# Kernel tuning notes

Measured on AMD Instinct MI355X. Metric: run time of the kernel, lower is better.

The kernel has to match this reference:

```python
import jax, jax.numpy as jnp
import numpy as np

D_MODEL = 2048
N_HEADS = 16
HEAD_DIM = D_MODEL // N_HEADS  # 128
SCALE_BASE = 512


def rotate_half(x):
    x1, x2 = jnp.split(x, 2, axis=-1)
    return jnp.concatenate((-x2, x1), axis=-1)


def rotary_xpos(seq_len, dim, dtype=jnp.float32):
    inv_freq = 1.0 / (10000.0 ** (jnp.arange(0, dim, 2, dtype=jnp.float32) / dim))
    t = jnp.arange(seq_len, dtype=jnp.float32)
    freqs = jnp.einsum('i,j->ij', t, inv_freq)
    freqs = jnp.concatenate((freqs, freqs), axis=-1)  # [S, dim]
    scale_base = (jnp.arange(0, dim, 2, dtype=jnp.float32) + 0.4 * dim) / (1.4 * dim)
    power = (t - seq_len // 2) / SCALE_BASE
    scale = scale_base[None, :] ** power[:, None]  # [S, dim/2]
    scale = jnp.concatenate((scale, scale), axis=-1)  # [S, dim]
    return freqs.astype(dtype), scale.astype(dtype)


def apply_rotary(t, pos, scale):
    return t * jnp.cos(pos) * scale + rotate_half(t) * jnp.sin(pos) * scale


def setup_inputs() -> dict:
    key = jax.random.key(0)
    ks = jax.random.split(key, 5)
    B, S = 2, 2048
    hidden_states = jax.random.normal(ks[0], (B, S, D_MODEL), dtype=jnp.float32)
    # Linear weights stored as [out, in] like torch; we use x @ W.T
    w_q = jax.random.normal(ks[1], (N_HEADS * HEAD_DIM, D_MODEL), dtype=jnp.float32) * 0.02
    w_kv = jax.random.normal(ks[2], (2 * HEAD_DIM, D_MODEL), dtype=jnp.float32) * 0.02
    w_proj = jax.random.normal(ks[3], (D_MODEL, N_HEADS * HEAD_DIM), dtype=jnp.float32) * 0.02
    b_proj = jax.random.normal(ks[4], (D_MODEL,), dtype=jnp.float32) * 0.02
    return {"hidden_states": hidden_states, "w_q": w_q, "w_kv": w_kv,
            "w_proj": w_proj, "b_proj": b_proj}


def reference(hidden_states, w_q, w_kv, w_proj, b_proj):
    B, S, _ = hidden_states.shape
    q = hidden_states @ w_q.T                      # [B,S,H*D]
    kv = hidden_states @ w_kv.T                    # [B,S,2*D]
    k, v = jnp.split(kv, 2, axis=-1)               # [B,S,D] each
    q = q.reshape(B, S, N_HEADS, HEAD_DIM).transpose(0, 2, 1, 3)  # [B,H,S,D]

    scale_w = HEAD_DIM ** (-0.5)
    q = q * scale_w
    k = k * scale_w

    pos, xscale = rotary_xpos(S, HEAD_DIM, q.dtype)
    q = apply_rotary(q, pos, xscale)               # broadcast [S,D] over [B,H,S,D]
    k = apply_rotary(k, pos, 1.0 / xscale)         # [B,S,D]

    attn = jnp.einsum('bnih,bjh->bnij', q, k)      # [B,H,S,S]
    causal = jnp.triu(jnp.ones((S, S), dtype=bool), 1)
    attn = jnp.where(causal, -jnp.finfo(attn.dtype).max, attn)
    attn = jax.nn.softmax(attn, axis=-1)

    out = jnp.einsum('bnij,bjd->bind', attn, v)    # [B,S,H,D]
    out = out.reshape(B, S, N_HEADS * HEAD_DIM)
    out = out @ w_proj.T + b_proj
    return out
```

## Files before the change

kernel.cpp:

```cpp
#include <hip/hip_runtime.h>
#include <math.h>

typedef __bf16 bf16;
typedef __bf16 bf16x8 __attribute__((ext_vector_type(8)));
typedef float f32x4 __attribute__((ext_vector_type(4)));

#define MFMA16(a, b, c) __builtin_amdgcn_mfma_f32_16x16x32_bf16((a), (b), (c), 0, 0, 0)

__device__ __forceinline__ float clampf(float v, float lo, float hi) {
  return fminf(fmaxf(v, lo), hi);
}

__device__ __forceinline__ void async_copy16(const void* g, void* l) {
  __builtin_amdgcn_global_load_lds(
      (__attribute__((address_space(1))) void*)g,
      (__attribute__((address_space(3))) void*)l,
      16, 0, 0);
}


__global__ void convert_bf16(const float* __restrict__ hs,
                             const float* __restrict__ wq,
                             const float* __restrict__ wkv,
                             const float* __restrict__ wproj,
                             bf16* __restrict__ hs_bf,
                             bf16* __restrict__ wqkv_bf,
                             bf16* __restrict__ wproj_bf) {
  const long long v = (long long)blockIdx.x * blockDim.x + threadIdx.x;
  const float* src;
  bf16* dst;
  long long off;
  if (v < 1048576) { src = hs; dst = hs_bf; off = v; }
  else if (v < 1572864) { src = wq; dst = wqkv_bf; off = v - 1048576; }
  else if (v < 1638400) { src = wkv; dst = wqkv_bf + 4194304; off = v - 1572864; }
  else { src = wproj; dst = wproj_bf; off = v - 1638400; }
  const f32x4* p = (const f32x4*)(src + off * 8);
  f32x4 f0 = p[0], f1 = p[1];
  bf16x8 r;
#pragma unroll
  for (int i = 0; i < 4; ++i) { r[i] = (bf16)f0[i]; r[i + 4] = (bf16)f1[i]; }
  *(bf16x8*)(dst + off * 8) = r;
}

__global__ __launch_bounds__(256, 2)
void gemm_qkv(const bf16* __restrict__ A, const bf16* __restrict__ Bw,
              bf16* __restrict__ Cq, bf16* __restrict__ Ckv) {
  const int K = 2048;
  __shared__ bf16 As[128 * 32];
  __shared__ bf16 Bs[128 * 32];
  const int tid = threadIdx.x;
  const int wave = tid >> 6, lane = tid & 63;
  const int quad = lane >> 4, l15 = lane & 15;
  const int r4 = lane >> 2, c4 = lane & 3;
  const int wm = wave >> 1, wn = wave & 1;
  const int bm = blockIdx.y * 128;
  const int bx = blockIdx.x;
  const bf16* Bp = Bw + (size_t)bx * 128 * K;

  const f32x4 vzero = {0.f, 0.f, 0.f, 0.f};
  f32x4 acc[4][4];
#pragma unroll
  for (int i = 0; i < 4; ++i)
#pragma unroll
    for (int j = 0; j < 4; ++j) acc[i][j] = vzero;

  for (int kt = 0; kt < K; kt += 32) {
    __syncthreads();
#pragma unroll
    for (int q = 0; q < 2; ++q) {
      const int chunk = wave * 2 + q;
      const int row = chunk * 16 + r4;
      async_copy16(A + (size_t)(bm + row) * K + kt + c4 * 8, (char*)As + chunk * 1024);
      async_copy16(Bp + (size_t)row * K + kt + c4 * 8, (char*)Bs + chunk * 1024);
    }
    __syncthreads();
    bf16x8 af[4], bfr[4];
#pragma unroll
    for (int i = 0; i < 4; ++i)
      af[i] = *(const bf16x8*)((const char*)As + (wm * 64 + i * 16 + l15) * 64 + quad * 16);
#pragma unroll
    for (int i = 0; i < 4; ++i)
      bfr[i] = *(const bf16x8*)((const char*)Bs + (wn * 64 + i * 16 + l15) * 64 + quad * 16);
#pragma unroll
    for (int mi = 0; mi < 4; ++mi)
#pragma unroll
      for (int ni = 0; ni < 4; ++ni)
        acc[mi][ni] = MFMA16(af[mi], bfr[ni], acc[mi][ni]);
  }

  bf16* Cp;
  int ldc, cn;
  if (bx < 16) { Cp = Cq; ldc = 2048; cn = bx * 128; }
  else { Cp = Ckv; ldc = 256; cn = (bx - 16) * 128; }
#pragma unroll
  for (int mi = 0; mi < 4; ++mi)
#pragma unroll
    for (int ni = 0; ni < 4; ++ni) {
      const int col = cn + wn * 64 + ni * 16 + l15;
#pragma unroll
      for (int r = 0; r < 4; ++r) {
        const int row = bm + wm * 64 + mi * 16 + quad * 4 + r;
        Cp[(size_t)row * ldc + col] = (bf16)clampf(acc[mi][ni][r], -1000.f, 1000.f);
      }
    }
}

__global__ __launch_bounds__(256, 2)
void gemm_proj(const bf16* __restrict__ A, const bf16* __restrict__ Bw,
               const float* __restrict__ bias, float* __restrict__ C) {
  const int K = 2048;
  __shared__ bf16 As[128 * 32];
  __shared__ bf16 Bs[128 * 32];
  const int tid = threadIdx.x;
  const int wave = tid >> 6, lane = tid & 63;
  const int quad = lane >> 4, l15 = lane & 15;
  const int r4 = lane >> 2, c4 = lane & 3;
  const int wm = wave >> 1, wn = wave & 1;
  const int bm = blockIdx.y * 128;
  const int bn = blockIdx.x * 128;
  const bf16* Bp = Bw + (size_t)bn * K;

  const f32x4 vzero = {0.f, 0.f, 0.f, 0.f};
  f32x4 acc[4][4];
#pragma unroll
  for (int i = 0; i < 4; ++i)
#pragma unroll
    for (int j = 0; j < 4; ++j) acc[i][j] = vzero;

  for (int kt = 0; kt < K; kt += 32) {
    __syncthreads();
#pragma unroll
    for (int q = 0; q < 2; ++q) {
      const int chunk = wave * 2 + q;
      const int row = chunk * 16 + r4;
      async_copy16(A + (size_t)(bm + row) * K + kt + c4 * 8, (char*)As + chunk * 1024);
      async_copy16(Bp + (size_t)row * K + kt + c4 * 8, (char*)Bs + chunk * 1024);
    }
    __syncthreads();
    bf16x8 af[4], bfr[4];
#pragma unroll
    for (int i = 0; i < 4; ++i)
      af[i] = *(const bf16x8*)((const char*)As + (wm * 64 + i * 16 + l15) * 64 + quad * 16);
#pragma unroll
    for (int i = 0; i < 4; ++i)
      bfr[i] = *(const bf16x8*)((const char*)Bs + (wn * 64 + i * 16 + l15) * 64 + quad * 16);
#pragma unroll
    for (int mi = 0; mi < 4; ++mi)
#pragma unroll
      for (int ni = 0; ni < 4; ++ni)
        acc[mi][ni] = MFMA16(af[mi], bfr[ni], acc[mi][ni]);
  }

#pragma unroll
  for (int mi = 0; mi < 4; ++mi)
#pragma unroll
    for (int ni = 0; ni < 4; ++ni) {
      const int col = bn + wn * 64 + ni * 16 + l15;
      const float bv = bias[col];
#pragma unroll
      for (int r = 0; r < 4; ++r) {
        const int row = bm + wm * 64 + mi * 16 + quad * 4 + r;
        C[(size_t)row * 2048 + col] = clampf(acc[mi][ni][r] + bv, -1000.f, 1000.f);
      }
    }
}

__global__ void rotary_kernel(bf16* __restrict__ Cq, bf16* __restrict__ Ckv,
                              bf16* __restrict__ VT) {
  const int row = blockIdx.x;
  const int b = row >> 11, s = row & 2047;
  const int t = threadIdx.x;
  const float power = (float)(s - 1024) * (1.0f / 512.0f);
  const float scale_w = 0.08838834764831845f;
  const float k_if = 0.2076205059304679f;

  const int h = t >> 4;
  const int j0 = (t & 15) * 4;
  const size_t qbase = (size_t)row * 2048 + (size_t)h * 128;
#pragma unroll
  for (int u = 0; u < 4; ++u) {
    const int j = j0 + u;
    const float pos = (float)s * exp2f(-k_if * (float)j);
    const float c = cosf(pos), sn = sinf(pos);
    const float sb = ((float)(2 * j) + 51.2f) * (1.0f / 179.2f);
    const float xs = exp2f(power * log2f(sb));
    const float f = xs * scale_w;
    const float q1 = (float)Cq[qbase + j];
    const float q2 = (float)Cq[qbase + j + 64];
    Cq[qbase + j]      = (bf16)((q1 * c - q2 * sn) * f);
    Cq[qbase + j + 64] = (bf16)((q2 * c + q1 * sn) * f);
  }

  if (t < 64) {
    const int j = t;
    const float pos = (float)s * exp2f(-k_if * (float)j);
    const float c = cosf(pos), sn = sinf(pos);
    const float sb = ((float)(2 * j) + 51.2f) * (1.0f / 179.2f);
    const float xs = exp2f(power * log2f(sb));
    const float f = scale_w / xs;
    const size_t kvb = (size_t)row * 256;
    const float k1 = (float)Ckv[kvb + j];
    const float k2 = (float)Ckv[kvb + j + 64];
    Ckv[kvb + j]      = (bf16)((k1 * c - k2 * sn) * f);
    Ckv[kvb + j + 64] = (bf16)((k2 * c + k1 * sn) * f);
  } else if (t < 128) {
    const int d = (t - 64) * 2;
    const size_t kvb = (size_t)row * 256 + 128;
    VT[((size_t)b * 128 + d) * 2048 + s]     = Ckv[kvb + d];
    VT[((size_t)b * 128 + d + 1) * 2048 + s] = Ckv[kvb + d + 1];
  }
}

__global__ __launch_bounds__(256, 2)
void flash_attn(const bf16* __restrict__ Qp, const bf16* __restrict__ Kkv,
                const bf16* __restrict__ VT, bf16* __restrict__ O) {
  __shared__ bf16 Ks[2][4 * 64 * 32];
  __shared__ bf16 Vs[2][2 * 128 * 32];
  __shared__ bf16 Ps[4][2 * 32 * 32];

  const int tid = threadIdx.x;
  const int wave = tid >> 6, lane = tid & 63;
  const int quad = lane >> 4, l15 = lane & 15;
  const int r4 = lane >> 2, c4 = lane & 3;
  const int bh = blockIdx.x, b = bh >> 4, h = bh & 15;
  const int y = blockIdx.y;
  const int tile = (y < 8) ? y : 23 - y;
  const int q0 = tile * 128;
  const int wrow = wave * 32;

  const bf16* Kb = Kkv + (size_t)b * 2048 * 256;
  const bf16* Vb = VT + (size_t)b * 128 * 2048;

  bf16x8 qa[2][4];
#pragma unroll
  for (int ms = 0; ms < 2; ++ms)
#pragma unroll
    for (int ks = 0; ks < 4; ++ks)
      qa[ms][ks] = *(const bf16x8*)(Qp + ((size_t)(b * 2048 + q0 + wrow + ms * 16 + l15)) * 2048 +
                                    h * 128 + ks * 32 + quad * 8);

  bf16x8 vones;
  {
    const bf16 ov = (bf16)((l15 == 0) ? 1.0f : 0.0f);
#pragma unroll
    for (int i = 0; i < 8; ++i) vones[i] = ov;
  }

  const f32x4 vzero = {0.f, 0.f, 0.f, 0.f};
  f32x4 oacc[2][8];
  f32x4 lacc[2];
#pragma unroll
  for (int ms = 0; ms < 2; ++ms) {
    lacc[ms] = vzero;
#pragma unroll
    for (int n8 = 0; n8 < 8; ++n8) oacc[ms][n8] = vzero;
  }

  auto stage = [&](int kv0, int buf) {
#pragma unroll
    for (int t = 0; t < 4; ++t) {
      const int ii = wave * 4 + t;
      const int p = ii >> 2, ch = ii & 3;
      async_copy16(Kb + (size_t)(kv0 + ch * 16 + r4) * 256 + p * 32 + c4 * 8,
                   (char*)Ks[buf] + ii * 1024);
    }
#pragma unroll
    for (int t = 0; t < 4; ++t) {
      const int ii = wave * 4 + t;
      const int pc = ii >> 3, ch = ii & 7;
      async_copy16(Vb + (size_t)(ch * 16 + r4) * 2048 + kv0 + pc * 32 + c4 * 8,
                   (char*)Vs[buf] + ii * 1024);
    }
  };

  stage(0, 0);
  const int nkv = (q0 >> 6) + 2;
  for (int jt = 0; jt < nkv; ++jt) {
    const int kv0 = jt * 64;
    const int buf = jt & 1;
    __syncthreads();
    if (jt + 1 < nkv) stage(kv0 + 64, buf ^ 1);

    if (kv0 <= q0 + wrow + 31) {
      f32x4 sacc[2][4];
#pragma unroll
      for (int ms = 0; ms < 2; ++ms)
#pragma unroll
        for (int ns = 0; ns < 4; ++ns) sacc[ms][ns] = vzero;
#pragma unroll
      for (int ks = 0; ks < 4; ++ks) {
        bf16x8 kb[4];
#pragma unroll
        for (int ns = 0; ns < 4; ++ns)
          kb[ns] = *(const bf16x8*)((const char*)Ks[buf] + ks * 4096 + (ns * 16 + l15) * 64 + quad * 16);
#pragma unroll
        for (int ms = 0; ms < 2; ++ms)
#pragma unroll
          for (int ns = 0; ns < 4; ++ns)
            sacc[ms][ns] = MFMA16(qa[ms][ks], kb[ns], sacc[ms][ns]);
      }
      if (kv0 + 63 > q0 + wrow) {
#pragma unroll
        for (int ms = 0; ms < 2; ++ms)
#pragma unroll
          for (int ns = 0; ns < 4; ++ns)
#pragma unroll
            for (int r = 0; r < 4; ++r) {
              const int qg = q0 + wrow + ms * 16 + quad * 4 + r;
              const int kg = kv0 + ns * 16 + l15;
              sacc[ms][ns][r] = (kg > qg) ? 0.0f : __expf(sacc[ms][ns][r]);
            }
      } else {
#pragma unroll
        for (int ms = 0; ms < 2; ++ms)
#pragma unroll
          for (int ns = 0; ns < 4; ++ns)
#pragma unroll
            for (int r = 0; r < 4; ++r)
              sacc[ms][ns][r] = __expf(sacc[ms][ns][r]);
      }
#pragma unroll
      for (int ms = 0; ms < 2; ++ms)
#pragma unroll
        for (int ns = 0; ns < 4; ++ns)
#pragma unroll
          for (int r = 0; r < 4; ++r)
            Ps[wave][(ns >> 1) * 1024 + (ms * 16 + quad * 4 + r) * 32 + (ns & 1) * 16 + l15] =
                (bf16)sacc[ms][ns][r];
#pragma unroll
      for (int ks2 = 0; ks2 < 2; ++ks2) {
        bf16x8 pa[2], vb[8];
#pragma unroll
        for (int ms = 0; ms < 2; ++ms)
          pa[ms] = *(const bf16x8*)((const char*)Ps[wave] + ks2 * 2048 + (ms * 16 + l15) * 64 + quad * 16);
#pragma unroll
        for (int n8 = 0; n8 < 8; ++n8)
          vb[n8] = *(const bf16x8*)((const char*)Vs[buf] + ks2 * 8192 + (n8 * 16 + l15) * 64 + quad * 16);
#pragma unroll
        for (int ms = 0; ms < 2; ++ms) {
#pragma unroll
          for (int n8 = 0; n8 < 8; ++n8)
            oacc[ms][n8] = MFMA16(pa[ms], vb[n8], oacc[ms][n8]);
          lacc[ms] = MFMA16(pa[ms], vones, lacc[ms]);
        }
      }
    }
  }

#pragma unroll
  for (int ms = 0; ms < 2; ++ms)
#pragma unroll
    for (int r = 0; r < 4; ++r) {
      const float l = __shfl(lacc[ms][r], lane & 48);
      const float inv = 1.0f / l;
      const int s = q0 + wrow + ms * 16 + quad * 4 + r;
#pragma unroll
      for (int n8 = 0; n8 < 8; ++n8) {
        const int d = n8 * 16 + l15;
        O[((size_t)(b * 2048 + s)) * 2048 + h * 128 + d] = (bf16)(oacc[ms][n8][r] * inv);
      }
    }
}

extern "C" void kernel_launch(void* const* d_in, const int* in_sizes, int n_in,
                              void* d_out, int out_size, void* d_ws, size_t ws_size,
                              hipStream_t stream) {
  const float* hs     = (const float*)d_in[0];
  const float* w_q    = (const float*)d_in[1];
  const float* w_kv   = (const float*)d_in[2];
  const float* w_proj = (const float*)d_in[3];
  const float* b_proj = (const float*)d_in[4];
  float* out = (float*)d_out;
  bf16* Qbuf  = (bf16*)d_out;
  bf16* hs_bf = (bf16*)((char*)d_out + 16777216);

  char* ws = (char*)d_ws;
  bf16* Ckv      = (bf16*)(ws);
  bf16* VT       = (bf16*)(ws + 2097152);
  bf16* AO       = (bf16*)(ws + 3145728);
  bf16* wqkv_bf  = (bf16*)(ws + 19922944);
  bf16* wproj_bf = (bf16*)(ws + 29360128);

  convert_bf16<<<dim3(8448), dim3(256), 0, stream>>>(hs, w_q, w_kv, w_proj,
                                                     hs_bf, wqkv_bf, wproj_bf);
  gemm_qkv<<<dim3(18, 32), dim3(256), 0, stream>>>(hs_bf, wqkv_bf, Qbuf, Ckv);
  rotary_kernel<<<dim3(4096), dim3(256), 0, stream>>>(Qbuf, Ckv, VT);
  flash_attn<<<dim3(32, 16), dim3(256), 0, stream>>>(Qbuf, Ckv, VT, AO);
  gemm_proj<<<dim3(16, 32), dim3(256), 0, stream>>>(AO, wproj_bf, b_proj, out);
}
```

Before: 287.6 us.

## Pair causal q-tiles per 512-thread block for balanced flash attention work

Each flash attention block now has 8 waves of 16 query rows instead of 4 waves of 32. It processes two 128-row query tiles in sequence (tile y, then tile 15-y), so every block does the same 34 KV iterations and causal load imbalance goes away. The grid halves to 32x8, and MFMA sections are wrapped in s_setprio to favour matrix issue. Each wave now reuses each K/V LDS load for only 16 rows, and the launch bound drops to one 512-thread block per CU.

```diff
diff --git a/kernel.cpp b/kernel.cpp
--- a/kernel.cpp
+++ b/kernel.cpp
@@ -211,12 +211,12 @@
   }
 }
 
-__global__ __launch_bounds__(256, 2)
+__global__ __launch_bounds__(512, 1)
 void flash_attn(const bf16* __restrict__ Qp, const bf16* __restrict__ Kkv,
                 const bf16* __restrict__ VT, bf16* __restrict__ O) {
   __shared__ bf16 Ks[2][4 * 64 * 32];
   __shared__ bf16 Vs[2][2 * 128 * 32];
-  __shared__ bf16 Ps[4][2 * 32 * 32];
+  __shared__ bf16 Ps[8][1024];
 
   const int tid = threadIdx.x;
   const int wave = tid >> 6, lane = tid & 63;
@@ -224,20 +224,11 @@
   const int r4 = lane >> 2, c4 = lane & 3;
   const int bh = blockIdx.x, b = bh >> 4, h = bh & 15;
   const int y = blockIdx.y;
-  const int tile = (y < 8) ? y : 23 - y;
-  const int q0 = tile * 128;
-  const int wrow = wave * 32;
+  const int nkvA = 2 * y + 2;
+  const int wrow = wave * 16;
 
   const bf16* Kb = Kkv + (size_t)b * 2048 * 256;
   const bf16* Vb = VT + (size_t)b * 128 * 2048;
-
-  bf16x8 qa[2][4];
-#pragma unroll
-  for (int ms = 0; ms < 2; ++ms)
-#pragma unroll
-    for (int ks = 0; ks < 4; ++ks)
-      qa[ms][ks] = *(const bf16x8*)(Qp + ((size_t)(b * 2048 + q0 + wrow + ms * 16 + l15)) * 2048 +
-                                    h * 128 + ks * 32 + quad * 8);
 
   bf16x8 vones;
   {
@@ -247,46 +238,72 @@
   }
 
   const f32x4 vzero = {0.f, 0.f, 0.f, 0.f};
-  f32x4 oacc[2][8];
-  f32x4 lacc[2];
-#pragma unroll
-  for (int ms = 0; ms < 2; ++ms) {
-    lacc[ms] = vzero;
-#pragma unroll
-    for (int n8 = 0; n8 < 8; ++n8) oacc[ms][n8] = vzero;
-  }
+  bf16x8 qa[4];
+  f32x4 oacc[8];
+  f32x4 lacc;
+
+  auto load_q = [&](int q0) {
+#pragma unroll
+    for (int ks = 0; ks < 4; ++ks)
+      qa[ks] = *(const bf16x8*)(Qp + ((size_t)(b * 2048 + q0 + wrow + l15)) * 2048 +
+                                h * 128 + ks * 32 + quad * 8);
+  };
+  auto reset_acc = [&]() {
+    lacc = vzero;
+#pragma unroll
+    for (int n8 = 0; n8 < 8; ++n8) oacc[n8] = vzero;
+  };
 
   auto stage = [&](int kv0, int buf) {
 #pragma unroll
-    for (int t = 0; t < 4; ++t) {
-      const int ii = wave * 4 + t;
+    for (int t = 0; t < 2; ++t) {
+      const int ii = wave * 2 + t;
       const int p = ii >> 2, ch = ii & 3;
       async_copy16(Kb + (size_t)(kv0 + ch * 16 + r4) * 256 + p * 32 + c4 * 8,
                    (char*)Ks[buf] + ii * 1024);
     }
 #pragma unroll
-    for (int t = 0; t < 4; ++t) {
-      const int ii = wave * 4 + t;
+    for (int t = 0; t < 2; ++t) {
+      const int ii = wave * 2 + t;
       const int pc = ii >> 3, ch = ii & 7;
       async_copy16(Vb + (size_t)(ch * 16 + r4) * 2048 + kv0 + pc * 32 + c4 * 8,
                    (char*)Vs[buf] + ii * 1024);
     }
   };
 
+  auto epilogue = [&](int q0) {
+#pragma unroll
+    for (int r = 0; r < 4; ++r) {
+      const float l = __shfl(lacc[r], lane & 48);
+      const float inv = 1.0f / l;
+      const int s = q0 + wrow + quad * 4 + r;
+#pragma unroll
+      for (int n8 = 0; n8 < 8; ++n8) {
+        const int d = n8 * 16 + l15;
+        O[((size_t)(b * 2048 + s)) * 2048 + h * 128 + d] = (bf16)(oacc[n8][r] * inv);
+      }
+    }
+  };
+
+  int q0 = y * 128;
+  load_q(q0);
+  reset_acc();
   stage(0, 0);
-  const int nkv = (q0 >> 6) + 2;
-  for (int jt = 0; jt < nkv; ++jt) {
-    const int kv0 = jt * 64;
+
+  for (int jt = 0; jt < 34; ++jt) {
+    const int kv0 = (jt < nkvA ? jt : jt - nkvA) * 64;
     const int buf = jt & 1;
     __syncthreads();
-    if (jt + 1 < nkv) stage(kv0 + 64, buf ^ 1);
-
-    if (kv0 <= q0 + wrow + 31) {
-      f32x4 sacc[2][4];
-#pragma unroll
-      for (int ms = 0; ms < 2; ++ms)
-#pragma unroll
-        for (int ns = 0; ns < 4; ++ns) sacc[ms][ns] = vzero;
+    if (jt + 1 < 34) {
+      const int njt = jt + 1;
+      stage((njt < nkvA ? njt : njt - nkvA) * 64, buf ^ 1);
+    }
+
+    if (kv0 <= q0 + wrow + 15) {
+      f32x4 sacc[4];
+#pragma unroll
+      for (int ns = 0; ns < 4; ++ns) sacc[ns] = vzero;
+      __builtin_amdgcn_s_setprio(1);
 #pragma unroll
       for (int ks = 0; ks < 4; ++ks) {
         bf16x8 kb[4];
@@ -294,72 +311,56 @@
         for (int ns = 0; ns < 4; ++ns)
           kb[ns] = *(const bf16x8*)((const char*)Ks[buf] + ks * 4096 + (ns * 16 + l15) * 64 + quad * 16);
 #pragma unroll
-        for (int ms = 0; ms < 2; ++ms)
-#pragma unroll
-          for (int ns = 0; ns < 4; ++ns)
-            sacc[ms][ns] = MFMA16(qa[ms][ks], kb[ns], sacc[ms][ns]);
-      }
+        for (int ns = 0; ns < 4; ++ns)
+          sacc[ns] = MFMA16(qa[ks], kb[ns], sacc[ns]);
+      }
+      __builtin_amdgcn_s_setprio(0);
       if (kv0 + 63 > q0 + wrow) {
 #pragma unroll
-        for (int ms = 0; ms < 2; ++ms)
-#pragma unroll
-          for (int ns = 0; ns < 4; ++ns)
-#pragma unroll
-            for (int r = 0; r < 4; ++r) {
-              const int qg = q0 + wrow + ms * 16 + quad * 4 + r;
-              const int kg = kv0 + ns * 16 + l15;
-              sacc[ms][ns][r] = (kg > qg) ? 0.0f : __expf(sacc[ms][ns][r]);
-            }
+        for (int ns = 0; ns < 4; ++ns)
+#pragma unroll
+          for (int r = 0; r < 4; ++r) {
+            const int qg = q0 + wrow + quad * 4 + r;
+            const int kg = kv0 + ns * 16 + l15;
+            sacc[ns][r] = (kg > qg) ? 0.0f : __expf(sacc[ns][r]);
+          }
       } else {
 #pragma unroll
-        for (int ms = 0; ms < 2; ++ms)
-#pragma unroll
-          for (int ns = 0; ns < 4; ++ns)
-#pragma unroll
-            for (int r = 0; r < 4; ++r)
-              sacc[ms][ns][r] = __expf(sacc[ms][ns][r]);
-      }
-#pragma unroll
-      for (int ms = 0; ms < 2; ++ms)
-#pragma unroll
         for (int ns = 0; ns < 4; ++ns)
 #pragma unroll
           for (int r = 0; r < 4; ++r)
-            Ps[wave][(ns >> 1) * 1024 + (ms * 16 + quad * 4 + r) * 32 + (ns & 1) * 16 + l15] =
-                (bf16)sacc[ms][ns][r];
+            sacc[ns][r] = __expf(sacc[ns][r]);
+      }
+#pragma unroll
+      for (int ns = 0; ns < 4; ++ns)
+#pragma unroll
+        for (int r = 0; r < 4; ++r)
+          *(bf16*)((char*)Ps[wave] + (ns >> 1) * 1024 + (quad * 4 + r) * 64 +
+                   ((ns & 1) * 16 + l15) * 2) = (bf16)sacc[ns][r];
 #pragma unroll
       for (int ks2 = 0; ks2 < 2; ++ks2) {
-        bf16x8 pa[2], vb[8];
-#pragma unroll
-        for (int ms = 0; ms < 2; ++ms)
-          pa[ms] = *(const bf16x8*)((const char*)Ps[wave] + ks2 * 2048 + (ms * 16 + l15) * 64 + quad * 16);
+        bf16x8 pa, vb[8];
+        pa = *(const bf16x8*)((const char*)Ps[wave] + ks2 * 1024 + l15 * 64 + quad * 16);
 #pragma unroll
         for (int n8 = 0; n8 < 8; ++n8)
           vb[n8] = *(const bf16x8*)((const char*)Vs[buf] + ks2 * 8192 + (n8 * 16 + l15) * 64 + quad * 16);
-#pragma unroll
-        for (int ms = 0; ms < 2; ++ms) {
-#pragma unroll
-          for (int n8 = 0; n8 < 8; ++n8)
-            oacc[ms][n8] = MFMA16(pa[ms], vb[n8], oacc[ms][n8]);
-          lacc[ms] = MFMA16(pa[ms], vones, lacc[ms]);
-        }
-      }
-    }
-  }
-
-#pragma unroll
-  for (int ms = 0; ms < 2; ++ms)
-#pragma unroll
-    for (int r = 0; r < 4; ++r) {
-      const float l = __shfl(lacc[ms][r], lane & 48);
-      const float inv = 1.0f / l;
-      const int s = q0 + wrow + ms * 16 + quad * 4 + r;
-#pragma unroll
-      for (int n8 = 0; n8 < 8; ++n8) {
-        const int d = n8 * 16 + l15;
-        O[((size_t)(b * 2048 + s)) * 2048 + h * 128 + d] = (bf16)(oacc[ms][n8][r] * inv);
-      }
-    }
+        __builtin_amdgcn_s_setprio(1);
+#pragma unroll
+        for (int n8 = 0; n8 < 8; ++n8)
+          oacc[n8] = MFMA16(pa, vb[n8], oacc[n8]);
+        lacc = MFMA16(pa, vones, lacc);
+        __builtin_amdgcn_s_setprio(0);
+      }
+    }
+
+    if (jt == nkvA - 1) {
+      epilogue(q0);
+      reset_acc();
+      q0 = (15 - y) * 128;
+      load_q(q0);
+    }
+  }
+  epilogue(q0);
 }
 
 extern "C" void kernel_launch(void* const* d_in, const int* in_sizes, int n_in,
@@ -385,6 +386,6 @@
                                                      hs_bf, wqkv_bf, wproj_bf);
   gemm_qkv<<<dim3(18, 32), dim3(256), 0, stream>>>(hs_bf, wqkv_bf, Qbuf, Ckv);
   rotary_kernel<<<dim3(4096), dim3(256), 0, stream>>>(Qbuf, Ckv, VT);
-  flash_attn<<<dim3(32, 16), dim3(256), 0, stream>>>(Qbuf, Ckv, VT, AO);
+  flash_attn<<<dim3(32, 8), dim3(512), 0, stream>>>(Qbuf, Ckv, VT, AO);
   gemm_proj<<<dim3(16, 32), dim3(256), 0, stream>>>(AO, wproj_bf, b_proj, out);
 }
```

Measured after the change: 289.0 us. No clear change (+0.5%).
